# Optimization experiments

Hardware: AMD Instinct MI355X
Metric: run time of the kernel (lower is better)

## Reference

```python
import jax, jax.numpy as jnp
import numpy as np

POOL = (7, 7)
IMAGE_SHAPE = (1024, 1024)  # image_meta image_shape in the original


def setup_inputs() -> dict:
    key = jax.random.key(0)
    ks = jax.random.split(key, 6)
    B, N, C = 2, 1000, 256
    yx = jax.random.uniform(ks[0], (B, N, 2), minval=0.0, maxval=0.7)
    hw = jax.random.uniform(ks[1], (B, N, 2), minval=0.02, maxval=0.3)
    boxes = jnp.concatenate([yx, jnp.clip(yx + hw, 0.0, 1.0)], axis=2)  # (y1,x1,y2,x2) normalized
    sizes = (256, 128, 64, 32)  # strides 4,8,16,32 on a 1024 image
    feats = {f"p{i+2}": jax.random.normal(ks[2 + i], (B, s, s, C), dtype=jnp.float32)
             for i, s in enumerate(sizes)}
    return {"boxes": boxes, **feats}


def _crop_and_resize(feat, boxes, pool_shape):
    # feat: [B,H,W,C], boxes: [B,N,4] normalized (y1,x1,y2,x2)
    B, H, W, C = feat.shape
    ph, pw = pool_shape
    y1, x1, y2, x2 = (boxes[..., i] for i in range(4))
    ty = jnp.linspace(0.0, 1.0, ph)
    tx = jnp.linspace(0.0, 1.0, pw)
    ys = (y1[..., None] + (y2 - y1)[..., None] * ty) * (H - 1)  # [B,N,ph]
    xs = (x1[..., None] + (x2 - x1)[..., None] * tx) * (W - 1)  # [B,N,pw]

    def per_image(f, ys_b, xs_b):
        y0f = jnp.floor(ys_b)
        x0f = jnp.floor(xs_b)
        wy = (ys_b - y0f)[:, :, None, None]  # [N,ph,1,1]
        wx = (xs_b - x0f)[:, None, :, None]  # [N,1,pw,1]
        y0 = jnp.clip(y0f, 0, H - 1).astype(jnp.int32)
        y1i = jnp.clip(y0f + 1, 0, H - 1).astype(jnp.int32)
        x0 = jnp.clip(x0f, 0, W - 1).astype(jnp.int32)
        x1i = jnp.clip(x0f + 1, 0, W - 1).astype(jnp.int32)
        # advanced indexing broadcasts [N,ph,1] x [N,1,pw] -> [N,ph,pw,C]
        v00 = f[y0[:, :, None], x0[:, None, :]]
        v01 = f[y0[:, :, None], x1i[:, None, :]]
        v10 = f[y1i[:, :, None], x0[:, None, :]]
        v11 = f[y1i[:, :, None], x1i[:, None, :]]
        top = v00 + wx * (v01 - v00)
        bot = v10 + wx * (v11 - v10)
        return top + wy * (bot - top)

    return jax.vmap(per_image)(feat, ys, xs)  # [B,N,ph,pw,C]


def reference(boxes, p2, p3, p4, p5):
    feats = (p2, p3, p4, p5)
    y1, x1, y2, x2 = (boxes[..., i] for i in range(4))
    h = y2 - y1
    w = x2 - x1
    image_area = float(IMAGE_SHAPE[0] * IMAGE_SHAPE[1])
    # FPN level assignment: log2(sqrt(hw) / (224/sqrt(area))), clamped to [2,5]
    roi_level = jnp.log2(jnp.sqrt(jnp.maximum(h * w, 1e-12)) / (224.0 / np.sqrt(image_area)))
    roi_level = jnp.clip(jnp.round(roi_level), 2, 5).astype(jnp.int32)  # [B,N]
    out = jnp.zeros(boxes.shape[:2] + POOL + (p2.shape[-1],), dtype=p2.dtype)
    for i, lvl in enumerate(range(2, 6)):
        pooled_l = _crop_and_resize(feats[i], boxes, POOL)  # [B,N,ph,pw,C]
        mask = (roi_level == lvl)[:, :, None, None, None]
        out = out + jnp.where(mask, pooled_l, 0.0)
    return out  # [B,N,ph,pw,C] in original box order
```

## Files before the change

kernel.cpp:

```cpp
#include <hip/hip_runtime.h>


#define NB 2
#define NN 1000
#define NC 256
#define PHW 7

__global__ __launch_bounds__(64) void roi_align_kernel(
    const float* __restrict__ boxes,
    const float* __restrict__ p2,
    const float* __restrict__ p3,
    const float* __restrict__ p4,
    const float* __restrict__ p5,
    float* __restrict__ out)
{
    const int cell = blockIdx.x;
    const int tid  = threadIdx.x;

    const int pxy = cell % 49;
    const int bn  = cell / 49;
    const int py  = pxy / 7;
    const int px  = pxy % 7;
    const int b   = bn / NN;

    const float* bx = boxes + (size_t)bn * 4;
    const float y1 = bx[0], x1 = bx[1], y2 = bx[2], x2 = bx[3];
    const float h = y2 - y1, w = x2 - x1;

    const float roi = log2f(sqrtf(fmaxf(h * w, 1e-12f)) * (1024.0f / 224.0f));
    int lvl = (int)rintf(roi);
    lvl = min(5, max(2, lvl));

    const float* feat;
    int H;
    switch (lvl) {
        case 2:  feat = p2; H = 256; break;
        case 3:  feat = p3; H = 128; break;
        case 4:  feat = p4; H = 64;  break;
        default: feat = p5; H = 32;  break;
    }
    const int W = H;

    const float ys = (y1 + h * ((float)py * (1.0f / 6.0f))) * (float)(H - 1);
    const float xs = (x1 + w * ((float)px * (1.0f / 6.0f))) * (float)(W - 1);
    const float y0f = floorf(ys), x0f = floorf(xs);
    const float wy = ys - y0f;
    const float wx = xs - x0f;
    const int y0 = min(H - 1, max(0, (int)y0f));
    const int yb = min(H - 1, max(0, (int)y0f + 1));
    const int x0 = min(W - 1, max(0, (int)x0f));
    const int xb = min(W - 1, max(0, (int)x0f + 1));

    const size_t base = (size_t)b * H * W * NC;
    const float4* r00 = (const float4*)(feat + base + ((size_t)y0 * W + x0) * NC);
    const float4* r01 = (const float4*)(feat + base + ((size_t)y0 * W + xb) * NC);
    const float4* r10 = (const float4*)(feat + base + ((size_t)yb * W + x0) * NC);
    const float4* r11 = (const float4*)(feat + base + ((size_t)yb * W + xb) * NC);

    const float4 v00 = r00[tid];
    const float4 v01 = r01[tid];
    const float4 v10 = r10[tid];
    const float4 v11 = r11[tid];

    float4 res;
    {
        float t, bo;
        t  = v00.x + wx * (v01.x - v00.x);
        bo = v10.x + wx * (v11.x - v10.x);
        res.x = t + wy * (bo - t);
        t  = v00.y + wx * (v01.y - v00.y);
        bo = v10.y + wx * (v11.y - v10.y);
        res.y = t + wy * (bo - t);
        t  = v00.z + wx * (v01.z - v00.z);
        bo = v10.z + wx * (v11.z - v10.z);
        res.z = t + wy * (bo - t);
        t  = v00.w + wx * (v01.w - v00.w);
        bo = v10.w + wx * (v11.w - v10.w);
        res.w = t + wy * (bo - t);
    }

    float4* o = (float4*)(out + (size_t)cell * NC);
    o[tid] = res;
}

extern "C" void kernel_launch(void* const* d_in, const int* in_sizes, int n_in,
                              void* d_out, int out_size, void* d_ws, size_t ws_size,
                              hipStream_t stream) {
    const float* boxes = (const float*)d_in[0];
    const float* p2    = (const float*)d_in[1];
    const float* p3    = (const float*)d_in[2];
    const float* p4    = (const float*)d_in[3];
    const float* p5    = (const float*)d_in[4];
    float* out = (float*)d_out;

    const int n_cells = NB * NN * PHW * PHW;
    roi_align_kernel<<<n_cells, 64, 0, stream>>>(boxes, p2, p3, p4, p5, out);
}
```

Measured before the change: 256.1 us.

## Process two cells per wave in 256-thread blocks with nontemporal output stores

Each block now runs four waves, and each wave handles two output cells. All eight corner loads are issued before any arithmetic, so more memory requests are in flight per wave and fewer blocks need to be launched. Output is written with nontemporal stores to keep the write-once result out of the cache, and the box read becomes a single vector load. The trade-off is higher register use and reliance on the cell count dividing evenly by 8, which holds here (98000/8).

```diff
diff --git a/kernel.cpp b/kernel.cpp
--- a/kernel.cpp
+++ b/kernel.cpp
@@ -4,27 +4,27 @@
 #define NB 2
 #define NN 1000
 #define NC 256
-#define PHW 7
+#define NCELLS (NB * NN * 49)
+#define CELLS_PER_BLOCK 8
 
-__global__ __launch_bounds__(64) void roi_align_kernel(
+typedef float vfloat4 __attribute__((ext_vector_type(4)));
+
+__device__ __forceinline__ void cell_setup(
+    int cell,
     const float* __restrict__ boxes,
-    const float* __restrict__ p2,
-    const float* __restrict__ p3,
-    const float* __restrict__ p4,
-    const float* __restrict__ p5,
-    float* __restrict__ out)
+    const float* __restrict__ p2, const float* __restrict__ p3,
+    const float* __restrict__ p4, const float* __restrict__ p5,
+    const vfloat4*& a00, const vfloat4*& a01, const vfloat4*& a10, const vfloat4*& a11,
+    float& wx, float& wy)
 {
-    const int cell = blockIdx.x;
-    const int tid  = threadIdx.x;
-
     const int pxy = cell % 49;
     const int bn  = cell / 49;
     const int py  = pxy / 7;
     const int px  = pxy % 7;
     const int b   = bn / NN;
 
-    const float* bx = boxes + (size_t)bn * 4;
-    const float y1 = bx[0], x1 = bx[1], y2 = bx[2], x2 = bx[3];
+    const vfloat4 bx = *(const vfloat4*)(boxes + (size_t)bn * 4);
+    const float y1 = bx.x, x1 = bx.y, y2 = bx.z, x2 = bx.w;
     const float h = y2 - y1, w = x2 - x1;
 
     const float roi = log2f(sqrtf(fmaxf(h * w, 1e-12f)) * (1024.0f / 224.0f));
@@ -44,43 +44,65 @@
     const float ys = (y1 + h * ((float)py * (1.0f / 6.0f))) * (float)(H - 1);
     const float xs = (x1 + w * ((float)px * (1.0f / 6.0f))) * (float)(W - 1);
     const float y0f = floorf(ys), x0f = floorf(xs);
-    const float wy = ys - y0f;
-    const float wx = xs - x0f;
+    wy = ys - y0f;
+    wx = xs - x0f;
     const int y0 = min(H - 1, max(0, (int)y0f));
     const int yb = min(H - 1, max(0, (int)y0f + 1));
     const int x0 = min(W - 1, max(0, (int)x0f));
     const int xb = min(W - 1, max(0, (int)x0f + 1));
 
     const size_t base = (size_t)b * H * W * NC;
-    const float4* r00 = (const float4*)(feat + base + ((size_t)y0 * W + x0) * NC);
-    const float4* r01 = (const float4*)(feat + base + ((size_t)y0 * W + xb) * NC);
-    const float4* r10 = (const float4*)(feat + base + ((size_t)yb * W + x0) * NC);
-    const float4* r11 = (const float4*)(feat + base + ((size_t)yb * W + xb) * NC);
+    a00 = (const vfloat4*)(feat + base + ((size_t)y0 * W + x0) * NC);
+    a01 = (const vfloat4*)(feat + base + ((size_t)y0 * W + xb) * NC);
+    a10 = (const vfloat4*)(feat + base + ((size_t)yb * W + x0) * NC);
+    a11 = (const vfloat4*)(feat + base + ((size_t)yb * W + xb) * NC);
+}
 
-    const float4 v00 = r00[tid];
-    const float4 v01 = r01[tid];
-    const float4 v10 = r10[tid];
-    const float4 v11 = r11[tid];
+__device__ __forceinline__ vfloat4 bilerp4(vfloat4 v00, vfloat4 v01, vfloat4 v10, vfloat4 v11,
+                                           float wx, float wy)
+{
+    vfloat4 top = v00 + wx * (v01 - v00);
+    vfloat4 bot = v10 + wx * (v11 - v10);
+    return top + wy * (bot - top);
+}
 
-    float4 res;
-    {
-        float t, bo;
-        t  = v00.x + wx * (v01.x - v00.x);
-        bo = v10.x + wx * (v11.x - v10.x);
-        res.x = t + wy * (bo - t);
-        t  = v00.y + wx * (v01.y - v00.y);
-        bo = v10.y + wx * (v11.y - v10.y);
-        res.y = t + wy * (bo - t);
-        t  = v00.z + wx * (v01.z - v00.z);
-        bo = v10.z + wx * (v11.z - v10.z);
-        res.z = t + wy * (bo - t);
-        t  = v00.w + wx * (v01.w - v00.w);
-        bo = v10.w + wx * (v11.w - v10.w);
-        res.w = t + wy * (bo - t);
-    }
+__global__ __launch_bounds__(256) void roi_align_kernel(
+    const float* __restrict__ boxes,
+    const float* __restrict__ p2,
+    const float* __restrict__ p3,
+    const float* __restrict__ p4,
+    const float* __restrict__ p5,
+    float* __restrict__ out)
+{
+    const int lane = threadIdx.x & 63;
+    const int wave = threadIdx.x >> 6;
 
-    float4* o = (float4*)(out + (size_t)cell * NC);
-    o[tid] = res;
+    const int c0 = (blockIdx.x * 4 + wave) * 2;
+    const int c1 = c0 + 1;
+
+    const vfloat4 *a00, *a01, *a10, *a11;
+    const vfloat4 *b00, *b01, *b10, *b11;
+    float wx0, wy0, wx1, wy1;
+
+    cell_setup(c0, boxes, p2, p3, p4, p5, a00, a01, a10, a11, wx0, wy0);
+    cell_setup(c1, boxes, p2, p3, p4, p5, b00, b01, b10, b11, wx1, wy1);
+
+    const vfloat4 va00 = a00[lane];
+    const vfloat4 va01 = a01[lane];
+    const vfloat4 va10 = a10[lane];
+    const vfloat4 va11 = a11[lane];
+    const vfloat4 vb00 = b00[lane];
+    const vfloat4 vb01 = b01[lane];
+    const vfloat4 vb10 = b10[lane];
+    const vfloat4 vb11 = b11[lane];
+
+    const vfloat4 r0 = bilerp4(va00, va01, va10, va11, wx0, wy0);
+    const vfloat4 r1 = bilerp4(vb00, vb01, vb10, vb11, wx1, wy1);
+
+    vfloat4* o0 = (vfloat4*)(out + (size_t)c0 * NC) + lane;
+    vfloat4* o1 = (vfloat4*)(out + (size_t)c1 * NC) + lane;
+    __builtin_nontemporal_store(r0, o0);
+    __builtin_nontemporal_store(r1, o1);
 }
 
 extern "C" void kernel_launch(void* const* d_in, const int* in_sizes, int n_in,
@@ -93,6 +115,6 @@
     const float* p5    = (const float*)d_in[4];
     float* out = (float*)d_out;
 
-    const int n_cells = NB * NN * PHW * PHW;
-    roi_align_kernel<<<n_cells, 64, 0, stream>>>(boxes, p2, p3, p4, p5, out);
+    const int n_blocks = NCELLS / CELLS_PER_BLOCK;
+    roi_align_kernel<<<n_blocks, 256, 0, stream>>>(boxes, p2, p3, p4, p5, out);
 }
```

After: 255.8 us. About the same (-0.1%).
